# Performance work log

Hardware: AMD Instinct MI355X
Metric: run time of the kernel (lower is better)

## Reference

```python
import jax, jax.numpy as jnp
import numpy as np

B, C, H, W = 4, 256, 128, 128
HEADS = 64
HD = C // HEADS  # 4
G = 32           # group norm groups
EPS = 1e-5


def setup_inputs() -> dict:
    key = jax.random.key(0)
    ks = jax.random.split(key, 6)
    x = jax.random.normal(ks[0], (B, C, H, W), dtype=jnp.float32)
    gn_weight = jnp.ones((1, C, 1, 1), dtype=jnp.float32)
    gn_bias = jnp.zeros((1, C, 1, 1), dtype=jnp.float32)
    # 1x1 convs stored as (out_ch, in_ch) matrices
    qkv_w = jax.random.normal(ks[1], (3 * C, C), dtype=jnp.float32) * 0.02
    qkv_b = jax.random.normal(ks[2], (3 * C,), dtype=jnp.float32) * 0.01
    out_w = jax.random.normal(ks[3], (C, C), dtype=jnp.float32) * 0.02
    out_b = jax.random.normal(ks[4], (C,), dtype=jnp.float32) * 0.01
    return {"x": x, "gn_weight": gn_weight, "gn_bias": gn_bias,
            "qkv_w": qkv_w, "qkv_b": qkv_b, "out_w": out_w, "out_b": out_b}


def group_norm(x, weight, bias):
    n, c, h, w = x.shape
    xg = x.reshape(n, G, -1)
    mean = xg.mean(axis=-1, keepdims=True)
    var = jnp.var(xg, axis=-1, keepdims=True, ddof=1)  # torch.var default is unbiased
    xg = (xg - mean) / jnp.sqrt(var + EPS)
    return xg.reshape(n, c, h, w) * weight + bias


def conv1x1(x, w, b):
    # x: (B, Cin, H, W), w: (Cout, Cin)
    return jnp.einsum('bchw,oc->bohw', x, w) + b[None, :, None, None]


def reference(x, gn_weight, gn_bias, qkv_w, qkv_b, out_w, out_b):
    skip = x
    h = group_norm(x, gn_weight, gn_bias)
    qkv = conv1x1(h, qkv_w, qkv_b)                      # (B, 3C, H, W)
    qkv = qkv.reshape(B, HEADS, 3 * HD, H * W)
    q, k, v = jnp.split(qkv, 3, axis=2)                  # each (B, heads, hd, HW)
    scores = jnp.einsum('bhdn,bhen->bhde', q, k) / (HD ** 0.5)  # (B, heads, hd, hd)
    scores = jax.nn.softmax(scores, axis=1)              # softmax over HEADS axis (as in source)
    out = jnp.einsum('bhde,bhen->bhdn', scores, v)       # (B, heads, hd, HW)
    out = out.reshape(B, C, H, W)
    out = conv1x1(out, out_w, out_b)
    return out + skip
```

## Files before the change

### kernel.cpp

```cpp
#include <hip/hip_runtime.h>


constexpr int kB = 4;
constexpr int kC = 256;
constexpr int kHW = 16384;
constexpr int kHeads = 64;
constexpr int kNG = 32;
constexpr int kCPG = 8;
constexpr int kCP1 = 257;
constexpr int kPS = 260;
constexpr float kEPS = 1e-5f;
constexpr int kNSplit = 32;

typedef __attribute__((ext_vector_type(8))) _Float16 f16x8;
typedef __attribute__((ext_vector_type(4))) _Float16 f16x4;
typedef __attribute__((ext_vector_type(4))) float f32x4;

union V8 { f16x8 v; uint4 u; _Float16 h[8]; };

constexpr size_t oXT    = 0;
constexpr size_t oXH    = oXT + (size_t)kB * kHW * kC / 2;
constexpr size_t oSpart = oXH + (size_t)kB * kHW * kC / 2;
constexpr size_t oS     = oSpart + (size_t)3 * kB * kNSplit * 128 * 128;
constexpr size_t oSums  = oS + (size_t)kB * kCP1 * kPS;
constexpr size_t oGv    = oSums + (size_t)kB * kC;
constexpr size_t oSc    = oGv + (size_t)kB * kC;
constexpr size_t oTc    = oSc + (size_t)kB * kC;
constexpr size_t oScore = oTc + (size_t)kB * kC;
constexpr size_t oAq    = oSpart;
constexpr size_t oM     = oXH;
constexpr size_t oGmH   = oXH + (size_t)kB * kC * kPS;

__global__ __launch_bounds__(256) void k0_tr(const float* __restrict__ x,
                                             _Float16* __restrict__ xT,
                                             _Float16* __restrict__ xH,
                                             float* __restrict__ sums) {
  const int nt = blockIdx.x, ct = blockIdx.y, b = blockIdx.z;
  __shared__ float T[64][65];
  __shared__ float psum[64][4];
  const float* xb = x + ((size_t)b * kC + ct * 64) * kHW + nt * 64;
  _Float16* xhb = xH + ((size_t)b * kC + ct * 64) * kHW + nt * 64;
  const int tid = threadIdx.x;

#pragma unroll
  for (int rep = 0; rep < 4; ++rep) {
    const int r = rep * 16 + (tid >> 4);
    const int c4 = (tid & 15) * 4;
    float4 v = *(const float4*)(xb + (size_t)r * kHW + c4);
    T[r][c4 + 0] = v.x; T[r][c4 + 1] = v.y; T[r][c4 + 2] = v.z; T[r][c4 + 3] = v.w;
    f16x4 hv = {(_Float16)v.x, (_Float16)v.y, (_Float16)v.z, (_Float16)v.w};
    *(f16x4*)(xhb + (size_t)r * kHW + c4) = hv;
  }
  __syncthreads();
  {
    const int q = tid >> 6, r = tid & 63;
    float s = 0.f;
#pragma unroll
    for (int i = 0; i < 16; ++i) s += T[r][q * 16 + i];
    psum[r][q] = s;
  }
  __syncthreads();
  if (tid < 64) {
    float s = psum[tid][0] + psum[tid][1] + psum[tid][2] + psum[tid][3];
    atomicAdd(&sums[b * kC + ct * 64 + tid], s);
  }
  const int nl = tid >> 2, cgrp = tid & 3;
  V8 lo, hi;
#pragma unroll
  for (int i = 0; i < 8; ++i)  lo.h[i] = (_Float16)T[cgrp * 16 + i][nl];
#pragma unroll
  for (int i = 0; i < 8; ++i)  hi.h[i] = (_Float16)T[cgrp * 16 + 8 + i][nl];
  _Float16* dst = xT + ((size_t)b * kHW + nt * 64 + nl) * kC + ct * 64 + cgrp * 16;
  *(uint4*)dst = lo.u;
  *(uint4*)(dst + 8) = hi.u;
}

__global__ __launch_bounds__(256) void k1_syrk(const _Float16* __restrict__ xH,
                                               float* __restrict__ Spart) {
  const int tt = blockIdx.x >> 5;
  const int sp = blockIdx.x & 31;
  const int b = blockIdx.y;
  const int ti = (tt == 2) ? 1 : 0;
  const int tj = (tt == 0) ? 0 : 1;
  const bool diag = (ti == tj);
  const _Float16* xb = xH + (size_t)b * kC * kHW;
  const int n0 = sp * (kHW / kNSplit);

  __shared__ __align__(16) _Float16 XI[128 * 64];
  __shared__ __align__(16) _Float16 XJ[128 * 64];

  const int tid = threadIdx.x;
  const int wave = tid >> 6, lane = tid & 63;
  const int wi = wave >> 1, wj = wave & 1;
  const int lrow = lane & 15, lgq = lane >> 4;

  f32x4 acc[16];
#pragma unroll
  for (int i = 0; i < 16; ++i) acc[i] = (f32x4){0.f, 0.f, 0.f, 0.f};

  for (int ch = 0; ch < kHW / kNSplit / 64; ++ch) {
    const int nb = n0 + ch * 64;
#pragma unroll
    for (int rep = 0; rep < 4; ++rep) {
      const int gi = tid + rep * 256;
      const int r = gi >> 3, g = gi & 7;
      const size_t boff = (size_t)r * 128 + (((unsigned)(g ^ (r & 7))) << 4);
      uint4 va = *(const uint4*)(xb + (size_t)(ti * 128 + r) * kHW + nb + g * 8);
      *(uint4*)((char*)XI + boff) = va;
      if (!diag) {
        uint4 vb = *(const uint4*)(xb + (size_t)(tj * 128 + r) * kHW + nb + g * 8);
        *(uint4*)((char*)XJ + boff) = vb;
      }
    }
    __syncthreads();
    const _Float16* XB = diag ? XI : XJ;
#pragma unroll
    for (int sub = 0; sub < 2; ++sub) {
      const int gq = sub * 4 + lgq;
      f16x8 afr[4], bfr[4];
#pragma unroll
      for (int ia = 0; ia < 4; ++ia) {
        const int r = wi * 64 + ia * 16 + lrow;
        afr[ia] = *(const f16x8*)((const char*)XI + (size_t)r * 128 + (((unsigned)(gq ^ (r & 7))) << 4));
      }
#pragma unroll
      for (int jb = 0; jb < 4; ++jb) {
        const int r = wj * 64 + jb * 16 + lrow;
        bfr[jb] = *(const f16x8*)((const char*)XB + (size_t)r * 128 + (((unsigned)(gq ^ (r & 7))) << 4));
      }
#pragma unroll
      for (int ia = 0; ia < 4; ++ia)
#pragma unroll
        for (int jb = 0; jb < 4; ++jb)
          acc[ia * 4 + jb] = __builtin_amdgcn_mfma_f32_16x16x32_f16(afr[ia], bfr[jb], acc[ia * 4 + jb], 0, 0, 0);
    }
    __syncthreads();
  }
  float* P = Spart + (((size_t)tt * kB + b) * kNSplit + sp) * 16384;
#pragma unroll
  for (int ia = 0; ia < 4; ++ia)
#pragma unroll
    for (int jb = 0; jb < 4; ++jb)
#pragma unroll
      for (int reg = 0; reg < 4; ++reg) {
        const int i = wi * 64 + ia * 16 + lgq * 4 + reg;
        const int j = wj * 64 + jb * 16 + lrow;
        P[(size_t)i * 128 + j] = acc[ia * 4 + jb][reg];
      }
}

__global__ __launch_bounds__(256) void k1r_reduce(const float* __restrict__ Spart,
                                                  float* __restrict__ S) {
  const int blk = blockIdx.x;
  const int tile12 = blk >> 4;
  const int part = blk & 15;
  const int tt = tile12 >> 2, b = tile12 & 3;
  const int rti = (tt == 2) ? 1 : 0;
  const int rtj = (tt == 0) ? 0 : 1;
  const int e0 = part * 1024 + threadIdx.x * 4;
  float4 s = {0.f, 0.f, 0.f, 0.f};
  const float* base = Spart + ((size_t)tt * kB + b) * kNSplit * 16384 + e0;
  for (int sp = 0; sp < kNSplit; ++sp) {
    float4 v = *(const float4*)(base + (size_t)sp * 16384);
    s.x += v.x; s.y += v.y; s.z += v.z; s.w += v.w;
  }
  const int i = e0 >> 7, j = e0 & 127;
  float* Sb = S + (size_t)b * kCP1 * kPS;
  float* dst = Sb + (size_t)(rti * 128 + i) * kPS + rtj * 128 + j;
  dst[0] = s.x; dst[1] = s.y; dst[2] = s.z; dst[3] = s.w;
  if (tt == 1) {
    Sb[(size_t)(128 + j + 0) * kPS + i] = s.x;
    Sb[(size_t)(128 + j + 1) * kPS + i] = s.y;
    Sb[(size_t)(128 + j + 2) * kPS + i] = s.z;
    Sb[(size_t)(128 + j + 3) * kPS + i] = s.w;
  }
}

__global__ __launch_bounds__(256) void k2a_stats(const float* __restrict__ S,
                                                 const float* __restrict__ sums,
                                                 const float* __restrict__ gw,
                                                 const float* __restrict__ gb,
                                                 float* __restrict__ sArr,
                                                 float* __restrict__ tArr) {
  const int b = blockIdx.x;
  const float* Sb = S + (size_t)b * kCP1 * kPS;
  __shared__ float sx[kC], sdg[kC], meanv[kNG], invv[kNG];
  const int c = threadIdx.x;
  sx[c]  = sums[b * kC + c];
  sdg[c] = Sb[(size_t)c * kPS + c];
  __syncthreads();
  if (c < kNG) {
    float sum = 0.f, ssq = 0.f;
    for (int k = 0; k < kCPG; ++k) { sum += sx[c * kCPG + k]; ssq += sdg[c * kCPG + k]; }
    const float n = (float)(kCPG * kHW);
    const float mean = sum / n;
    const float var = (ssq - n * mean * mean) / (n - 1.0f);
    meanv[c] = mean;
    invv[c] = rsqrtf(var + kEPS);
  }
  __syncthreads();
  const int g = c / kCPG;
  const float s = gw[c] * invv[g];
  sArr[b * kC + c] = s;
  tArr[b * kC + c] = gb[c] - meanv[g] * s;
}

__global__ __launch_bounds__(256) void k3a_aq(const float* __restrict__ S,
                                              const float* __restrict__ sums,
                                              const float* __restrict__ sArr,
                                              const float* __restrict__ tArr,
                                              const float* __restrict__ qkv_w,
                                              const float* __restrict__ qkv_b,
                                              float* __restrict__ Aq) {
  const int ct = blockIdx.x, mt = blockIdx.y, b = blockIdx.z;
  const float* Sb = S + (size_t)b * kCP1 * kPS;
  const float HWf = (float)kHW;
  __shared__ float Wt[32][68];
  __shared__ float Gs[32][68];
  __shared__ float shs[kC], sht[kC], shx[kC], shr[kC];
  const int tid = threadIdx.x;
  {
    const float sv = sArr[b * kC + tid];
    const float tv = tArr[b * kC + tid];
    const float xv = sums[b * kC + tid];
    shs[tid] = sv; sht[tid] = tv; shx[tid] = xv;
    shr[tid] = sv * xv + tv * HWf;
  }
  __syncthreads();
  float acc[16];
#pragma unroll
  for (int i = 0; i < 16; ++i) acc[i] = 0.f;
  const int i0 = (tid & 15) * 4;
  const int j0 = (tid >> 4) * 4;
  const int cp0 = ct * 64;

  for (int cb = 0; cb < kC; cb += 32) {
    int idx = tid;
#pragma unroll
    for (int r = 0; r < 2; ++r) {
      const int m = idx >> 3;
      const int c4 = (idx & 7) * 4;
      const int mg = mt * 64 + m;
      const int row = 12 * (mg >> 2) + (mg & 3);
      float4 v = *(const float4*)(qkv_w + (size_t)row * kC + cb + c4);
      Wt[c4 + 0][m] = v.x; Wt[c4 + 1][m] = v.y; Wt[c4 + 2][m] = v.z; Wt[c4 + 3][m] = v.w;
      idx += 256;
    }
    idx = tid;
#pragma unroll
    for (int r = 0; r < 2; ++r) {
      const int cc = idx >> 4;
      const int n4 = (idx & 15) * 4;
      const int rr = cb + cc;
      const float s_r = shs[rr], t_r = sht[rr], x_r = shx[rr];
      float4 o;
      if (cp0 + n4 < kC) {
        float4 v = *(const float4*)(Sb + (size_t)rr * kPS + cp0 + n4);
        const int cp = cp0 + n4;
        o.x = s_r * (shs[cp + 0] * v.x + sht[cp + 0] * x_r) + t_r * shr[cp + 0];
        o.y = s_r * (shs[cp + 1] * v.y + sht[cp + 1] * x_r) + t_r * shr[cp + 1];
        o.z = s_r * (shs[cp + 2] * v.z + sht[cp + 2] * x_r) + t_r * shr[cp + 2];
        o.w = s_r * (shs[cp + 3] * v.w + sht[cp + 3] * x_r) + t_r * shr[cp + 3];
      } else if (cp0 + n4 == kC) {
        o = (float4){s_r * x_r + t_r * HWf, 0.f, 0.f, 0.f};
      } else {
        o = (float4){0.f, 0.f, 0.f, 0.f};
      }
      *(float4*)&Gs[cc][n4] = o;
      idx += 256;
    }
    __syncthreads();
#pragma unroll
    for (int kk = 0; kk < 32; ++kk) {
      float4 a = *(const float4*)&Wt[kk][i0];
      float4 g = *(const float4*)&Gs[kk][j0];
      acc[0]  += a.x * g.x; acc[1]  += a.x * g.y; acc[2]  += a.x * g.z; acc[3]  += a.x * g.w;
      acc[4]  += a.y * g.x; acc[5]  += a.y * g.y; acc[6]  += a.y * g.z; acc[7]  += a.y * g.w;
      acc[8]  += a.z * g.x; acc[9]  += a.z * g.y; acc[10] += a.z * g.z; acc[11] += a.z * g.w;
      acc[12] += a.w * g.x; acc[13] += a.w * g.y; acc[14] += a.w * g.z; acc[15] += a.w * g.w;
    }
    __syncthreads();
  }
#pragma unroll
  for (int mi = 0; mi < 4; ++mi) {
    const int mg = mt * 64 + i0 + mi;
    const float bias = qkv_b[12 * (mg >> 2) + (mg & 3)];
#pragma unroll
    for (int cj = 0; cj < 4; ++cj) {
      const int cp = cp0 + j0 + cj;
      if (cp < kCP1) {
        const float g256 = (cp < kC) ? shr[cp] : HWf;
        Aq[((size_t)b * kC + mg) * kCP1 + cp] = acc[mi * 4 + cj] + bias * g256;
      }
    }
  }
}

__global__ __launch_bounds__(256) void k3b_scores(const float* __restrict__ Aq,
                                                  const float* __restrict__ qkv_w,
                                                  const float* __restrict__ qkv_b,
                                                  float* __restrict__ score) {
  const int h = blockIdx.x, b = blockIdx.y;
  const int tid = threadIdx.x, wave = tid >> 6, lane = tid & 63;
#pragma unroll
  for (int p = wave; p < 16; p += 4) {
    const int d = p >> 2, e = p & 3;
    const float* aqr = Aq + ((size_t)b * kC + h * 4 + d) * kCP1;
    const int krow = h * 12 + 4 + e;
    float s = 0.f;
#pragma unroll
    for (int it = 0; it < 4; ++it) {
      const int cp = lane + it * 64;
      s += aqr[cp] * qkv_w[(size_t)krow * kC + cp];
    }
    if (lane == 0) s += aqr[256] * qkv_b[krow];
#pragma unroll
    for (int off = 32; off; off >>= 1) s += __shfl_xor(s, off);
    if (lane == 0) score[((size_t)(b * kHeads) + h) * 16 + p] = 0.5f * s;
  }
}

__global__ __launch_bounds__(256) void k45_M(const float* __restrict__ score,
                                             const float* __restrict__ qkv_w,
                                             const float* __restrict__ qkv_b,
                                             float* __restrict__ M) {
  const int b = blockIdx.y;
  const int cidx = blockIdx.x;
  const int h = cidx >> 2, d = cidx & 3;
  __shared__ float sc[64][4];
  __shared__ float mx[4], sm[4];
  const int tid = threadIdx.x;
  {
    const int h2 = tid >> 2, e = tid & 3;
    sc[h2][e] = score[((size_t)(b * kHeads) + h2) * 16 + d * 4 + e];
  }
  __syncthreads();
  const int wave = tid >> 6, lane = tid & 63;
  {
    const float v = sc[lane][wave];
    float m = v;
#pragma unroll
    for (int off = 32; off; off >>= 1) m = fmaxf(m, __shfl_xor(m, off));
    float e2 = expf(v - m);
#pragma unroll
    for (int off = 32; off; off >>= 1) e2 += __shfl_xor(e2, off);
    if (lane == 0) { mx[wave] = m; sm[wave] = e2; }
  }
  __syncthreads();
  const float p0 = expf(sc[h][0] - mx[0]) / sm[0];
  const float p1 = expf(sc[h][1] - mx[1]) / sm[1];
  const float p2 = expf(sc[h][2] - mx[2]) / sm[2];
  const float p3 = expf(sc[h][3] - mx[3]) / sm[3];
  for (int cp = tid; cp < kCP1; cp += 256) {
    float a;
    if (cp < kC) {
      a = p0 * qkv_w[(size_t)(h * 12 + 8 + 0) * kC + cp] +
          p1 * qkv_w[(size_t)(h * 12 + 8 + 1) * kC + cp] +
          p2 * qkv_w[(size_t)(h * 12 + 8 + 2) * kC + cp] +
          p3 * qkv_w[(size_t)(h * 12 + 8 + 3) * kC + cp];
    } else {
      a = p0 * qkv_b[h * 12 + 8 + 0] + p1 * qkv_b[h * 12 + 8 + 1] +
          p2 * qkv_b[h * 12 + 8 + 2] + p3 * qkv_b[h * 12 + 8 + 3];
    }
    M[((size_t)b * kC + cidx) * kPS + cp] = a;
  }
}

__global__ __launch_bounds__(256) void k5b_gemm(const float* __restrict__ M,
                                                const float* __restrict__ out_w,
                                                const float* __restrict__ sArr,
                                                const float* __restrict__ tArr,
                                                _Float16* __restrict__ GmH,
                                                float* __restrict__ gvec) {
  const int ct = blockIdx.x, ot = blockIdx.y, b = blockIdx.z;
  const float* Mb = M + (size_t)b * kC * kPS;
  __shared__ float Wt[32][68];
  __shared__ float Gs[32][68];
  __shared__ float gred[64][17];
  float acc[16];
#pragma unroll
  for (int i = 0; i < 16; ++i) acc[i] = 0.f;
  const int tid = threadIdx.x;
  const int i0 = (tid & 15) * 4;
  const int j0 = (tid >> 4) * 4;
  const int cp0 = ct * 64;

  for (int cb = 0; cb < kC; cb += 32) {
    int idx = tid;
#pragma unroll
    for (int r = 0; r < 2; ++r) {
      const int m = idx >> 3;
      const int c4 = (idx & 7) * 4;
      float4 v = *(const float4*)(out_w + (size_t)(ot * 64 + m) * kC + cb + c4);
      Wt[c4 + 0][m] = v.x; Wt[c4 + 1][m] = v.y; Wt[c4 + 2][m] = v.z; Wt[c4 + 3][m] = v.w;
      idx += 256;
    }
    idx = tid;
#pragma unroll
    for (int r = 0; r < 2; ++r) {
      const int cc = idx >> 4;
      const int n4 = (idx & 15) * 4;
      float4 v = {0.f, 0.f, 0.f, 0.f};
      if (cp0 + n4 < kCP1) v = *(const float4*)(Mb + (size_t)(cb + cc) * kPS + cp0 + n4);
      *(float4*)&Gs[cc][n4] = v;
      idx += 256;
    }
    __syncthreads();
#pragma unroll
    for (int kk = 0; kk < 32; ++kk) {
      float4 a = *(const float4*)&Wt[kk][i0];
      float4 g = *(const float4*)&Gs[kk][j0];
      acc[0]  += a.x * g.x; acc[1]  += a.x * g.y; acc[2]  += a.x * g.z; acc[3]  += a.x * g.w;
      acc[4]  += a.y * g.x; acc[5]  += a.y * g.y; acc[6]  += a.y * g.z; acc[7]  += a.y * g.w;
      acc[8]  += a.z * g.x; acc[9]  += a.z * g.y; acc[10] += a.z * g.z; acc[11] += a.z * g.w;
      acc[12] += a.w * g.x; acc[13] += a.w * g.y; acc[14] += a.w * g.z; acc[15] += a.w * g.w;
    }
    __syncthreads();
  }
  float gpart[4] = {0.f, 0.f, 0.f, 0.f};
#pragma unroll
  for (int mi = 0; mi < 4; ++mi) {
    const int o = ot * 64 + i0 + mi;
#pragma unroll
    for (int cj = 0; cj < 4; ++cj) {
      const int cp = cp0 + j0 + cj;
      const float f = acc[mi * 4 + cj];
      if (cp < kC) {
        GmH[((size_t)b * kC + o) * kC + cp] = (_Float16)(f * sArr[b * kC + cp]);
        gpart[mi] += f * tArr[b * kC + cp];
      } else if (cp == kC) {
        gpart[mi] += f;
      }
    }
  }
#pragma unroll
  for (int mi = 0; mi < 4; ++mi) gred[i0 + mi][tid >> 4] = gpart[mi];
  __syncthreads();
  if (tid < 64) {
    float s = 0.f;
#pragma unroll
    for (int k = 0; k < 16; ++k) s += gred[tid][k];
    atomicAdd(&gvec[b * kC + ot * 64 + tid], s);
  }
}

__global__ __launch_bounds__(256) void k6_final(const _Float16* __restrict__ xT,
                                                const _Float16* __restrict__ GmH,
                                                const float* __restrict__ gvec,
                                                const float* __restrict__ out_b,
                                                const float* __restrict__ x,
                                                float* __restrict__ out) {
  const int nt = blockIdx.x, ot = blockIdx.y, b = blockIdx.z;
  __shared__ __align__(16) char smem[64 * 132 * 4];
  _Float16* GT = (_Float16*)smem;
  _Float16* XT = (_Float16*)(smem + 16384);
  float* Ep = (float*)smem;
  const int tid = threadIdx.x;
  const int wave = tid >> 6, lane = tid & 63;
  const int wo = wave >> 1, wn = wave & 1;
  const int lrow = lane & 15, lgq = lane >> 4;

  f32x4 acc[16];
#pragma unroll
  for (int i = 0; i < 16; ++i) acc[i] = (f32x4){0.f, 0.f, 0.f, 0.f};

  for (int cc = 0; cc < kC; cc += 64) {
#pragma unroll
    for (int rep = 0; rep < 4; ++rep) {
      const int gi = tid + rep * 256;
      const int r = gi >> 3, g = gi & 7;
      const size_t boff = (size_t)r * 128 + (((unsigned)(g ^ (r & 7))) << 4);
      uint4 gv = *(const uint4*)(GmH + ((size_t)(b * kC + ot * 128 + r)) * kC + cc + g * 8);
      *(uint4*)((char*)GT + boff) = gv;
      uint4 xv = *(const uint4*)(xT + ((size_t)b * kHW + nt * 128 + r) * kC + cc + g * 8);
      *(uint4*)((char*)XT + boff) = xv;
    }
    __syncthreads();
#pragma unroll
    for (int sub = 0; sub < 2; ++sub) {
      const int gq = sub * 4 + lgq;
      f16x8 afr[4], bfr[4];
#pragma unroll
      for (int ia = 0; ia < 4; ++ia) {
        const int r = wo * 64 + ia * 16 + lrow;
        afr[ia] = *(const f16x8*)((const char*)GT + (size_t)r * 128 + (((unsigned)(gq ^ (r & 7))) << 4));
      }
#pragma unroll
      for (int jb = 0; jb < 4; ++jb) {
        const int r = wn * 64 + jb * 16 + lrow;
        bfr[jb] = *(const f16x8*)((const char*)XT + (size_t)r * 128 + (((unsigned)(gq ^ (r & 7))) << 4));
      }
#pragma unroll
      for (int ia = 0; ia < 4; ++ia)
#pragma unroll
        for (int jb = 0; jb < 4; ++jb)
          acc[ia * 4 + jb] = __builtin_amdgcn_mfma_f32_16x16x32_f16(afr[ia], bfr[jb], acc[ia * 4 + jb], 0, 0, 0);
    }
    __syncthreads();
  }
#pragma unroll
  for (int p = 0; p < 2; ++p) {
    if (wo == p) {
#pragma unroll
      for (int ia = 0; ia < 4; ++ia)
#pragma unroll
        for (int jb = 0; jb < 4; ++jb)
#pragma unroll
          for (int reg = 0; reg < 4; ++reg)
            Ep[(size_t)(ia * 16 + lgq * 4 + reg) * 132 + wn * 64 + jb * 16 + lrow] =
                acc[ia * 4 + jb][reg];
    }
    __syncthreads();
#pragma unroll
    for (int it = 0; it < 8; ++it) {
      const int id = it * 256 + tid;
      const int row = id >> 5, nc = (id & 31) * 4;
      const int o = ot * 128 + p * 64 + row;
      const float gvv = gvec[b * kC + o] + out_b[o];
      float4 e = *(const float4*)&Ep[(size_t)row * 132 + nc];
      const size_t gidx = ((size_t)b * kC + o) * kHW + nt * 128 + nc;
      float4 sk = *(const float4*)&x[gidx];
      float4 res = {e.x + gvv + sk.x, e.y + gvv + sk.y, e.z + gvv + sk.z, e.w + gvv + sk.w};
      *(float4*)&out[gidx] = res;
    }
    __syncthreads();
  }
}

extern "C" void kernel_launch(void* const* d_in, const int* in_sizes, int n_in,
                              void* d_out, int out_size, void* d_ws, size_t ws_size,
                              hipStream_t stream) {
  const float* x    = (const float*)d_in[0];
  const float* gnw  = (const float*)d_in[1];
  const float* gnb  = (const float*)d_in[2];
  const float* qkvw = (const float*)d_in[3];
  const float* qkvb = (const float*)d_in[4];
  const float* outw = (const float*)d_in[5];
  const float* outb = (const float*)d_in[6];
  float* out = (float*)d_out;
  float* ws = (float*)d_ws;

  _Float16* xT   = (_Float16*)(ws + oXT);
  _Float16* xH   = (_Float16*)(ws + oXH);
  float* Spart   = ws + oSpart;
  float* S       = ws + oS;
  float* sums    = ws + oSums;
  float* gv      = ws + oGv;
  float* sArr    = ws + oSc;
  float* tArr    = ws + oTc;
  float* score   = ws + oScore;
  float* Aq      = ws + oAq;
  float* M       = ws + oM;
  _Float16* GmH  = (_Float16*)(ws + oGmH);

  hipMemsetAsync(sums, 0, (size_t)2 * kB * kC * sizeof(float), stream);
  k0_tr<<<dim3(kHW / 64, kC / 64, kB), 256, 0, stream>>>(x, xT, xH, sums);
  k1_syrk<<<dim3(3 * kNSplit, kB), 256, 0, stream>>>(xH, Spart);
  k1r_reduce<<<dim3(3 * kB * 16), 256, 0, stream>>>(Spart, S);
  k2a_stats<<<kB, 256, 0, stream>>>(S, sums, gnw, gnb, sArr, tArr);
  k3a_aq<<<dim3(5, 4, kB), 256, 0, stream>>>(S, sums, sArr, tArr, qkvw, qkvb, Aq);
  k3b_scores<<<dim3(kHeads, kB), 256, 0, stream>>>(Aq, qkvw, qkvb, score);
  k45_M<<<dim3(kC, kB), 256, 0, stream>>>(score, qkvw, qkvb, M);
  k5b_gemm<<<dim3(5, 4, kB), 256, 0, stream>>>(M, outw, sArr, tArr, GmH, gv);
  k6_final<<<dim3(kHW / 128, kC / 128, kB), 256, 0, stream>>>(xT, GmH, gv, outb, x, out);
}
```

Measured before the change: 238.4 us.

## Double-buffer SYRK and final GEMM tiles with async global-to-LDS loads

Both the SYRK partial-product kernel and the final output GEMM now stage their tiles with global_load_lds direct-to-LDS copies into two buffers, so the next chunk is prefetched while MFMAs run on the current one. The LDS write pattern is rearranged so each wave writes contiguous 8-row groups while keeping the XOR swizzle on the source side. In the final kernel, the small GmH weight operand is read straight from global memory rather than through LDS. The aim is to hide load latency and drop the register round trip, at the cost of more LDS per block and uncoalesced direct global reads for the A operand. The loop's trailing sync and any wait on the async loads are not visible, so ordering between buffers is uncertain.

Measured after the change: 243.4 us. 1.02x slower.

```diff
diff --git a/kernel.cpp b/kernel.cpp
--- a/kernel.cpp
+++ b/kernel.cpp
@@ -17,6 +17,12 @@
 typedef __attribute__((ext_vector_type(4))) float f32x4;
 
 union V8 { f16x8 v; uint4 u; _Float16 h[8]; };
+
+__device__ __forceinline__ void gload16(const void* g, void* l) {
+  __builtin_amdgcn_global_load_lds(
+      (const __attribute__((address_space(1))) void*)g,
+      (__attribute__((address_space(3))) void*)l, 16, 0, 0);
+}
 
 constexpr size_t oXT    = 0;
 constexpr size_t oXH    = oXT + (size_t)kB * kHW * kC / 2;
@@ -86,34 +92,45 @@
   const _Float16* xb = xH + (size_t)b * kC * kHW;
   const int n0 = sp * (kHW / kNSplit);
 
-  __shared__ __align__(16) _Float16 XI[128 * 64];
-  __shared__ __align__(16) _Float16 XJ[128 * 64];
+  __shared__ __align__(16) _Float16 XI[2][128 * 64];
+  __shared__ __align__(16) _Float16 XJ[2][128 * 64];
 
   const int tid = threadIdx.x;
   const int wave = tid >> 6, lane = tid & 63;
   const int wi = wave >> 1, wj = wave & 1;
   const int lrow = lane & 15, lgq = lane >> 4;
+  const int srow = lane >> 3, sslot = lane & 7;
+
+  const _Float16* srcI = xb + (size_t)(ti * 128) * kHW + n0;
+  const _Float16* srcJ = xb + (size_t)(tj * 128) * kHW + n0;
 
   f32x4 acc[16];
 #pragma unroll
   for (int i = 0; i < 16; ++i) acc[i] = (f32x4){0.f, 0.f, 0.f, 0.f};
 
-  for (int ch = 0; ch < kHW / kNSplit / 64; ++ch) {
-    const int nb = n0 + ch * 64;
+  auto stage = [&](int buf, int nb) {
 #pragma unroll
     for (int rep = 0; rep < 4; ++rep) {
-      const int gi = tid + rep * 256;
-      const int r = gi >> 3, g = gi & 7;
-      const size_t boff = (size_t)r * 128 + (((unsigned)(g ^ (r & 7))) << 4);
-      uint4 va = *(const uint4*)(xb + (size_t)(ti * 128 + r) * kHW + nb + g * 8);
-      *(uint4*)((char*)XI + boff) = va;
+      const int rr = rep * 32 + wave * 8 + srow;
+      const int g = sslot ^ (rr & 7);
+      char* dI = (char*)XI[buf] + (rep * 32 + wave * 8) * 128;
+      gload16(srcI + (size_t)rr * kHW + nb + g * 8, dI);
       if (!diag) {
-        uint4 vb = *(const uint4*)(xb + (size_t)(tj * 128 + r) * kHW + nb + g * 8);
-        *(uint4*)((char*)XJ + boff) = vb;
-      }
-    }
-    __syncthreads();
-    const _Float16* XB = diag ? XI : XJ;
+        char* dJ = (char*)XJ[buf] + (rep * 32 + wave * 8) * 128;
+        gload16(srcJ + (size_t)rr * kHW + nb + g * 8, dJ);
+      }
+    }
+  };
+
+  stage(0, 0);
+  __syncthreads();
+
+  constexpr int NCH = kHW / kNSplit / 64;
+  for (int ch = 0; ch < NCH; ++ch) {
+    const int buf = ch & 1;
+    if (ch + 1 < NCH) stage(buf ^ 1, (ch + 1) * 64);
+    const _Float16* XIb = XI[buf];
+    const _Float16* XBb = diag ? XI[buf] : XJ[buf];
 #pragma unroll
     for (int sub = 0; sub < 2; ++sub) {
       const int gq = sub * 4 + lgq;
@@ -121,12 +138,12 @@
 #pragma unroll
       for (int ia = 0; ia < 4; ++ia) {
         const int r = wi * 64 + ia * 16 + lrow;
-        afr[ia] = *(const f16x8*)((const char*)XI + (size_t)r * 128 + (((unsigned)(gq ^ (r & 7))) << 4));
+        afr[ia] = *(const f16x8*)((const char*)XIb + (size_t)r * 128 + (((unsigned)(gq ^ (r & 7))) << 4));
       }
 #pragma unroll
       for (int jb = 0; jb < 4; ++jb) {
         const int r = wj * 64 + jb * 16 + lrow;
-        bfr[jb] = *(const f16x8*)((const char*)XB + (size_t)r * 128 + (((unsigned)(gq ^ (r & 7))) << 4));
+        bfr[jb] = *(const f16x8*)((const char*)XBb + (size_t)r * 128 + (((unsigned)(gq ^ (r & 7))) << 4));
       }
 #pragma unroll
       for (int ia = 0; ia < 4; ++ia)
@@ -452,30 +469,38 @@
                                                 float* __restrict__ out) {
   const int nt = blockIdx.x, ot = blockIdx.y, b = blockIdx.z;
   __shared__ __align__(16) char smem[64 * 132 * 4];
-  _Float16* GT = (_Float16*)smem;
-  _Float16* XT = (_Float16*)(smem + 16384);
   float* Ep = (float*)smem;
   const int tid = threadIdx.x;
   const int wave = tid >> 6, lane = tid & 63;
   const int wo = wave >> 1, wn = wave & 1;
   const int lrow = lane & 15, lgq = lane >> 4;
+  const int srow = lane >> 3, sslot = lane & 7;
+
+  const _Float16* xrow = xT + ((size_t)b * kHW + nt * 128) * kC;
+  const _Float16* Grow = GmH + (size_t)(b * kC + ot * 128) * kC;
+
+  auto stage = [&](int buf, int cc) {
+#pragma unroll
+    for (int rep = 0; rep < 4; ++rep) {
+      const int rr = rep * 32 + wave * 8 + srow;
+      const int g = sslot ^ (rr & 7);
+      gload16(xrow + (size_t)rr * kC + cc + g * 8,
+              smem + buf * 16384 + (rep * 32 + wave * 8) * 128);
+    }
+  };
 
   f32x4 acc[16];
 #pragma unroll
   for (int i = 0; i < 16; ++i) acc[i] = (f32x4){0.f, 0.f, 0.f, 0.f};
 
-  for (int cc = 0; cc < kC; cc += 64) {
-#pragma unroll
-    for (int rep = 0; rep < 4; ++rep) {
-      const int gi = tid + rep * 256;
-      const int r = gi >> 3, g = gi & 7;
-      const size_t boff = (size_t)r * 128 + (((unsigned)(g ^ (r & 7))) << 4);
-      uint4 gv = *(const uint4*)(GmH + ((size_t)(b * kC + ot * 128 + r)) * kC + cc + g * 8);
-      *(uint4*)((char*)GT + boff) = gv;
-      uint4 xv = *(const uint4*)(xT + ((size_t)b * kHW + nt * 128 + r) * kC + cc + g * 8);
-      *(uint4*)((char*)XT + boff) = xv;
-    }
-    __syncthreads();
+  stage(0, 0);
+  __syncthreads();
+
+  for (int ci = 0; ci < 4; ++ci) {
+    const int cc = ci * 64;
+    const int buf = ci & 1;
+    if (ci < 3) stage(buf ^ 1, cc + 64);
+    const char* XB = smem + buf * 16384;
 #pragma unroll
     for (int sub = 0; sub < 2; ++sub) {
       const int gq = sub * 4 + lgq;
@@ -483,12 +508,12 @@
 #pragma unroll
       for (int ia = 0; ia < 4; ++ia) {
         const int r = wo * 64 + ia * 16 + lrow;
-        afr[ia] = *(const f16x8*)((const char*)GT + (size_t)r * 128 + (((unsigned)(gq ^ (r & 7))) << 4));
+        afr[ia] = *(const f16x8*)(Grow + (size_t)r * kC + cc + gq * 8);
       }
 #pragma unroll
       for (int jb = 0; jb < 4; ++jb) {
         const int r = wn * 64 + jb * 16 + lrow;
-        bfr[jb] = *(const f16x8*)((const char*)XT + (size_t)r * 128 + (((unsigned)(gq ^ (r & 7))) << 4));
+        bfr[jb] = *(const f16x8*)(XB + (size_t)r * 128 + (((unsigned)(gq ^ (r & 7))) << 4));
       }
 #pragma unroll
       for (int ia = 0; ia < 4; ++ia)
```
